# Kernel optimization log

Hardware: AMD Instinct MI355X
Metric: run time of the kernel (lower is better)

## Reference

```python
import jax, jax.numpy as jnp
import numpy as np

# AlphaFold2-scale config
C_S, C_Z, H, D = 256, 128, 8, 32
T = H * D  # total_dim = 256
B, S, N = 1, 128, 256  # batch, MSA rows, residues
EPS = 1e-5
SCALE = 1.0 / np.sqrt(D).astype(np.float32)


def _layer_norm(x, w, b):
    m = jnp.mean(x, axis=-1, keepdims=True)
    v = jnp.var(x, axis=-1, keepdims=True)
    return (x - m) * jax.lax.rsqrt(v + EPS) * w + b


def setup_inputs() -> dict:
    key = jax.random.key(0)
    ks = jax.random.split(key, 8)
    w = lambda k, shape: jax.random.normal(k, shape, dtype=jnp.float32) * 0.02
    return {
        "msa_representation": jax.random.normal(ks[0], (B, S, N, C_S), dtype=jnp.float32),
        "pair_representation": jax.random.normal(ks[1], (B, N, N, C_Z), dtype=jnp.float32),
        "ln_msa_w": jnp.ones((C_S,), jnp.float32),
        "ln_msa_b": jnp.zeros((C_S,), jnp.float32),
        "ln_pair_w": jnp.ones((C_Z,), jnp.float32),
        "ln_pair_b": jnp.zeros((C_Z,), jnp.float32),
        "Wq": w(ks[2], (C_S, T)),
        "Wk": w(ks[3], (C_S, T)),
        "Wv": w(ks[4], (C_S, T)),
        "Wpair": w(ks[5], (C_Z, H)),
        "Wg": w(ks[6], (C_S, T)),
        "bg": jnp.zeros((T,), jnp.float32),
        "Wo": w(ks[7], (T, C_S)),
        "bo": jnp.zeros((C_S,), jnp.float32),
    }


def reference(msa_representation, pair_representation, ln_msa_w, ln_msa_b,
              ln_pair_w, ln_pair_b, Wq, Wk, Wv, Wpair, Wg, bg, Wo, bo):
    msa = _layer_norm(msa_representation, ln_msa_w, ln_msa_b)  # [B,S,N,C_S]
    q = (msa @ Wq).reshape(B, S, N, H, D)
    k = (msa @ Wk).reshape(B, S, N, H, D)
    v = (msa @ Wv).reshape(B, S, N, H, D)
    g = jax.nn.sigmoid(msa @ Wg + bg).reshape(B, S, N, H, D)

    pair = _layer_norm(pair_representation, ln_pair_w, ln_pair_b)  # [B,N,N,C_Z]
    bias = jnp.transpose(pair @ Wpair, (0, 3, 1, 2))[:, None]  # [B,1,H,N,N]

    scores = jnp.einsum('bsihd,bsjhd->bshij', q, k) * SCALE + bias  # [B,S,H,N,N]
    attn = jax.nn.softmax(scores, axis=-1)
    vals = jnp.einsum('bshij,bsjhd->bsihd', attn, v)  # [B,S,N,H,D]
    vals = (g * vals).reshape(B, S, N, T)
    return vals @ Wo + bo  # [B,S,N,C_S]
```

## Files before the change

### kernel.cpp

```cpp
#include <hip/hip_runtime.h>

typedef unsigned short u16;
typedef unsigned int u32;
typedef __bf16 bf16x8 __attribute__((ext_vector_type(8)));
typedef float f32x4 __attribute__((ext_vector_type(4)));

#define EPS 1e-5f
#define SCALE 0.17677669529663687f

__device__ __forceinline__ u16 f2bf(float f) {
  u32 u = __builtin_bit_cast(u32, f);
  u32 r = (u + 0x7fffu + ((u >> 16) & 1u)) >> 16;
  return (u16)r;
}
__device__ __forceinline__ float bf2f(u16 v) {
  return __builtin_bit_cast(float, (u32)v << 16);
}
__device__ __forceinline__ u32 pack2(float a, float b) {
  return (u32)f2bf(a) | ((u32)f2bf(b) << 16);
}

__global__ __launch_bounds__(256) void k_ln_msa(const float* __restrict__ x,
                                                const float* __restrict__ w,
                                                const float* __restrict__ b,
                                                u16* __restrict__ y) {
  int wid = threadIdx.x >> 6, lane = threadIdx.x & 63;
  long row = (long)blockIdx.x * 4 + wid;
  const float4 v = *reinterpret_cast<const float4*>(x + row * 256 + lane * 4);
  float s = v.x + v.y + v.z + v.w;
  float ss = v.x * v.x + v.y * v.y + v.z * v.z + v.w * v.w;
#pragma unroll
  for (int off = 1; off < 64; off <<= 1) {
    s += __shfl_xor(s, off);
    ss += __shfl_xor(ss, off);
  }
  float m = s * (1.0f / 256.0f);
  float var = ss * (1.0f / 256.0f) - m * m;
  float rs = rsqrtf(var + EPS);
  int c = lane * 4;
  u16 o0 = f2bf((v.x - m) * rs * w[c + 0] + b[c + 0]);
  u16 o1 = f2bf((v.y - m) * rs * w[c + 1] + b[c + 1]);
  u16 o2 = f2bf((v.z - m) * rs * w[c + 2] + b[c + 2]);
  u16 o3 = f2bf((v.w - m) * rs * w[c + 3] + b[c + 3]);
  uint2 pk;
  pk.x = (u32)o0 | ((u32)o1 << 16);
  pk.y = (u32)o2 | ((u32)o3 << 16);
  *reinterpret_cast<uint2*>(y + row * 256 + c) = pk;
}

__global__ __launch_bounds__(256) void k_pair_bias(const float* __restrict__ x,
                                                   const float* __restrict__ w,
                                                   const float* __restrict__ b,
                                                   const float* __restrict__ Wp,
                                                   float* __restrict__ bias) {
  int wid = threadIdx.x >> 6, lane = threadIdx.x & 63;
  long row = (long)blockIdx.x * 4 + wid;
  const float2 v = *reinterpret_cast<const float2*>(x + row * 128 + lane * 2);
  float s = v.x + v.y, ss = v.x * v.x + v.y * v.y;
#pragma unroll
  for (int off = 1; off < 64; off <<= 1) {
    s += __shfl_xor(s, off);
    ss += __shfl_xor(ss, off);
  }
  float m = s * (1.0f / 128.0f);
  float var = ss * (1.0f / 128.0f) - m * m;
  float rs = rsqrtf(var + EPS);
  int c = lane * 2;
  float x0 = (v.x - m) * rs * w[c] + b[c];
  float x1 = (v.y - m) * rs * w[c + 1] + b[c + 1];
  const float4* wp = reinterpret_cast<const float4*>(Wp + (long)c * 8);
  float4 a0 = wp[0], a1 = wp[1], a2 = wp[2], a3 = wp[3];
  float p[8];
  p[0] = x0 * a0.x + x1 * a2.x; p[1] = x0 * a0.y + x1 * a2.y;
  p[2] = x0 * a0.z + x1 * a2.z; p[3] = x0 * a0.w + x1 * a2.w;
  p[4] = x0 * a1.x + x1 * a3.x; p[5] = x0 * a1.y + x1 * a3.y;
  p[6] = x0 * a1.z + x1 * a3.z; p[7] = x0 * a1.w + x1 * a3.w;
#pragma unroll
  for (int off = 1; off < 64; off <<= 1) {
#pragma unroll
    for (int h = 0; h < 8; h++) p[h] += __shfl_xor(p[h], off);
  }
  if (lane == 0) {
#pragma unroll
    for (int h = 0; h < 8; h++) bias[(long)h * 65536 + row] = p[h];
  }
}

__global__ __launch_bounds__(256) void k_prep_w(const float* __restrict__ Wq,
                                                const float* __restrict__ Wk,
                                                const float* __restrict__ Wv,
                                                const float* __restrict__ Wg,
                                                const float* __restrict__ Wo,
                                                u16* __restrict__ Wt,
                                                u16* __restrict__ WoT) {
  int tid = blockIdx.x * 256 + threadIdx.x;
  if (tid < 262144) {
    int n = tid >> 8, kk = tid & 255;
    int sel = n >> 8, c = n & 255;
    const float* W = (sel == 0) ? Wq : (sel == 1) ? Wk : (sel == 2) ? Wv : Wg;
    float v = W[kk * 256 + c];
    if (sel == 0) v *= SCALE;
    Wt[tid] = f2bf(v);
  } else {
    int t = tid - 262144;
    int n = t >> 8, kk = t & 255;
    WoT[t] = f2bf(Wo[kk * 256 + n]);
  }
}

__global__ __launch_bounds__(256) void k_proj(const u16* __restrict__ X,
                                              const u16* __restrict__ Wt,
                                              const float* __restrict__ bg,
                                              u16* __restrict__ qkg,
                                              u16* __restrict__ vt) {
  __shared__ u16 Bs[128 * 256];
  int tid = threadIdx.x;
  int wid = tid >> 6, lane = tid & 63;
  int lr = lane & 15, lg = lane >> 4;
  int m0 = blockIdx.x * 128;
  int n0 = blockIdx.y * 128;
  int sel = n0 >> 8;

#pragma unroll
  for (int i = 0; i < 16; i++) {
    int u = i * 256 + tid;
    int n = u >> 5, cu = u & 31;
    uint4 xw = *reinterpret_cast<const uint4*>(Wt + (long)(n0 + n) * 256 + cu * 8);
    *reinterpret_cast<uint4*>(&Bs[n * 256 + ((cu ^ (n & 7)) * 8)]) = xw;
  }
  __syncthreads();

  int mw = m0 + wid * 32;
  bf16x8 a[2][8];
#pragma unroll
  for (int mi = 0; mi < 2; mi++)
#pragma unroll
    for (int kk = 0; kk < 8; kk++)
      a[mi][kk] = *reinterpret_cast<const bf16x8*>(
          X + (long)(mw + mi * 16 + lr) * 256 + kk * 32 + lg * 8);

  f32x4 acc[2][8];
#pragma unroll
  for (int mi = 0; mi < 2; mi++)
#pragma unroll
    for (int ni = 0; ni < 8; ni++) acc[mi][ni] = (f32x4){0.f, 0.f, 0.f, 0.f};

#pragma unroll
  for (int ni = 0; ni < 8; ni++) {
    bf16x8 bfr[8];
#pragma unroll
    for (int kk = 0; kk < 8; kk++)
      bfr[kk] = *reinterpret_cast<const bf16x8*>(
          &Bs[(ni * 16 + lr) * 256 + (((kk * 4 + lg) ^ (lr & 7)) * 8)]);
#pragma unroll
    for (int kk = 0; kk < 8; kk++) {
      acc[0][ni] = __builtin_amdgcn_mfma_f32_16x16x32_bf16(a[0][kk], bfr[kk], acc[0][ni], 0, 0, 0);
      acc[1][ni] = __builtin_amdgcn_mfma_f32_16x16x32_bf16(a[1][kk], bfr[kk], acc[1][ni], 0, 0, 0);
    }
  }

  int s = m0 >> 8;
  if (sel == 2) {
#pragma unroll
    for (int ni = 0; ni < 8; ni++) {
      int cq = (n0 & 255) + ni * 16 + lr;
      int hh = cq >> 5, dd = cq & 31;
      u16* vbase = vt + (((long)s * 8 + hh) * 32 + dd) * 256;
#pragma unroll
      for (int mi = 0; mi < 2; mi++) {
        int i = (m0 & 255) + wid * 32 + mi * 16 + lg * 4;
        uint2 pk;
        pk.x = pack2(acc[mi][ni][0], acc[mi][ni][1]);
        pk.y = pack2(acc[mi][ni][2], acc[mi][ni][3]);
        *reinterpret_cast<uint2*>(vbase + i) = pk;
      }
    }
  } else {
    int t = (sel == 3) ? 2 : sel;
#pragma unroll
    for (int ni = 0; ni < 8; ni++) {
      int cq = (n0 & 255) + ni * 16 + lr;
      int hh = cq >> 5, dd = cq & 31;
      float bgv = (sel == 3) ? bg[cq] : 0.f;
      u16* qbase = qkg + (long)(t * 8 + hh) * 32768 * 32;
#pragma unroll
      for (int mi = 0; mi < 2; mi++) {
#pragma unroll
        for (int r = 0; r < 4; r++) {
          int row = m0 + wid * 32 + mi * 16 + lg * 4 + r;
          float val = acc[mi][ni][r];
          if (sel == 3) val = 1.0f / (1.0f + __expf(-(val + bgv)));
          qbase[(long)row * 32 + dd] = f2bf(val);
        }
      }
    }
  }
}

__global__ __launch_bounds__(256) void k_attn(const u16* __restrict__ qkg,
                                              const u16* __restrict__ vt,
                                              const float* __restrict__ bias,
                                              u16* __restrict__ vals) {
  __shared__ alignas(16) u16 VTs[32 * 272];
  __shared__ alignas(16) u16 Plds[4][16 * 272];
  int tid = threadIdx.x;
  int wid = tid >> 6, lane = tid & 63;
  int lr = lane & 15, lg = lane >> 4;
  int i0 = blockIdx.x * 64, h = blockIdx.y, s = blockIdx.z;

  const u16* qb = qkg + ((long)(0 + h) * 32768 + s * 256) * 32;
  const u16* kb = qkg + ((long)(8 + h) * 32768 + s * 256) * 32;
  const u16* gb = qkg + ((long)(16 + h) * 32768 + s * 256) * 32;
  const u16* vb = vt + ((long)s * 8 + h) * 32 * 256;

#pragma unroll
  for (int k = 0; k < 4; k++) {
    int c = tid + k * 256;
    uint4 u = *reinterpret_cast<const uint4*>(vb + c * 8);
    int d = c >> 5, p = c & 31;
    *reinterpret_cast<uint4*>(&VTs[d * 272 + p * 8]) = u;
  }
  __syncthreads();

  int iw0 = i0 + wid * 16;
  bf16x8 qf = *reinterpret_cast<const bf16x8*>(qb + (long)(iw0 + lr) * 32 + lg * 8);

  f32x4 p[16];
#pragma unroll
  for (int jt = 0; jt < 16; jt++) {
    bf16x8 kf = *reinterpret_cast<const bf16x8*>(kb + (long)(jt * 16 + lr) * 32 + lg * 8);
    f32x4 z = (f32x4){0.f, 0.f, 0.f, 0.f};
    p[jt] = __builtin_amdgcn_mfma_f32_16x16x32_bf16(kf, qf, z, 0, 0, 0);
  }

  const float4* bp4 = reinterpret_cast<const float4*>(bias + (long)h * 65536 + (long)(iw0 + lr) * 256);
  float sum = 0.f;
#pragma unroll
  for (int jt = 0; jt < 16; jt++) {
    float4 bv = bp4[jt * 4 + lg];
    float e0 = __expf(p[jt][0] + bv.x);
    float e1 = __expf(p[jt][1] + bv.y);
    float e2 = __expf(p[jt][2] + bv.z);
    float e3 = __expf(p[jt][3] + bv.w);
    sum += (e0 + e1) + (e2 + e3);
    uint2 pk;
    pk.x = pack2(e0, e1);
    pk.y = pack2(e2, e3);
    *reinterpret_cast<uint2*>(&Plds[wid][lr * 272 + jt * 16 + lg * 4]) = pk;
  }
  sum += __shfl_xor(sum, 16);
  sum += __shfl_xor(sum, 32);

  f32x4 o[2];
  o[0] = (f32x4){0.f, 0.f, 0.f, 0.f};
  o[1] = (f32x4){0.f, 0.f, 0.f, 0.f};
#pragma unroll
  for (int ks = 0; ks < 8; ks++) {
    bf16x8 pa = *reinterpret_cast<const bf16x8*>(&Plds[wid][lr * 272 + ks * 32 + lg * 8]);
#pragma unroll
    for (int nt = 0; nt < 2; nt++) {
      bf16x8 vf = *reinterpret_cast<const bf16x8*>(&VTs[(nt * 16 + lr) * 272 + ks * 32 + lg * 8]);
      o[nt] = __builtin_amdgcn_mfma_f32_16x16x32_bf16(pa, vf, o[nt], 0, 0, 0);
    }
  }

  float inv = 1.0f / sum;
#pragma unroll
  for (int r = 0; r < 4; r++) {
    float invr = __shfl(inv, lg * 4 + r);
    int row = iw0 + lg * 4 + r;
#pragma unroll
    for (int nt = 0; nt < 2; nt++) {
      int d = nt * 16 + lr;
      float gv = bf2f(gb[(long)row * 32 + d]);
      float ov = o[nt][r] * invr * gv;
      vals[((long)s * 256 + row) * 256 + h * 32 + d] = f2bf(ov);
    }
  }
}

__global__ __launch_bounds__(256) void k_out(const u16* __restrict__ X,
                                             const u16* __restrict__ WoT,
                                             const float* __restrict__ bo,
                                             float* __restrict__ out) {
  __shared__ u16 Bs[128 * 256];
  int tid = threadIdx.x;
  int wid = tid >> 6, lane = tid & 63;
  int lr = lane & 15, lg = lane >> 4;
  int m0 = blockIdx.x * 128;
  int n0 = blockIdx.y * 128;

#pragma unroll
  for (int i = 0; i < 16; i++) {
    int u = i * 256 + tid;
    int n = u >> 5, cu = u & 31;
    uint4 xw = *reinterpret_cast<const uint4*>(WoT + (long)(n0 + n) * 256 + cu * 8);
    *reinterpret_cast<uint4*>(&Bs[n * 256 + ((cu ^ (n & 7)) * 8)]) = xw;
  }
  __syncthreads();

  int mw = m0 + wid * 32;
  bf16x8 a[2][8];
#pragma unroll
  for (int mi = 0; mi < 2; mi++)
#pragma unroll
    for (int kk = 0; kk < 8; kk++)
      a[mi][kk] = *reinterpret_cast<const bf16x8*>(
          X + (long)(mw + mi * 16 + lr) * 256 + kk * 32 + lg * 8);

  f32x4 acc[2][8];
#pragma unroll
  for (int mi = 0; mi < 2; mi++)
#pragma unroll
    for (int ni = 0; ni < 8; ni++) acc[mi][ni] = (f32x4){0.f, 0.f, 0.f, 0.f};

#pragma unroll
  for (int ni = 0; ni < 8; ni++) {
    bf16x8 bfr[8];
#pragma unroll
    for (int kk = 0; kk < 8; kk++)
      bfr[kk] = *reinterpret_cast<const bf16x8*>(
          &Bs[(ni * 16 + lr) * 256 + (((kk * 4 + lg) ^ (lr & 7)) * 8)]);
#pragma unroll
    for (int kk = 0; kk < 8; kk++) {
      acc[0][ni] = __builtin_amdgcn_mfma_f32_16x16x32_bf16(a[0][kk], bfr[kk], acc[0][ni], 0, 0, 0);
      acc[1][ni] = __builtin_amdgcn_mfma_f32_16x16x32_bf16(a[1][kk], bfr[kk], acc[1][ni], 0, 0, 0);
    }
  }

#pragma unroll
  for (int ni = 0; ni < 8; ni++) {
    int col = n0 + ni * 16 + lr;
    float bias_c = bo[col];
#pragma unroll
    for (int mi = 0; mi < 2; mi++) {
#pragma unroll
      for (int r = 0; r < 4; r++) {
        int row = m0 + wid * 32 + mi * 16 + lg * 4 + r;
        out[(long)row * 256 + col] = acc[mi][ni][r] + bias_c;
      }
    }
  }
}

extern "C" void kernel_launch(void* const* d_in, const int* in_sizes, int n_in,
                              void* d_out, int out_size, void* d_ws, size_t ws_size,
                              hipStream_t stream) {
  (void)in_sizes; (void)n_in; (void)out_size; (void)ws_size;
  const float* msa = (const float*)d_in[0];
  const float* pair = (const float*)d_in[1];
  const float* ln_msa_w = (const float*)d_in[2];
  const float* ln_msa_b = (const float*)d_in[3];
  const float* ln_pair_w = (const float*)d_in[4];
  const float* ln_pair_b = (const float*)d_in[5];
  const float* Wq = (const float*)d_in[6];
  const float* Wk = (const float*)d_in[7];
  const float* Wv = (const float*)d_in[8];
  const float* Wpair = (const float*)d_in[9];
  const float* Wg = (const float*)d_in[10];
  const float* bg = (const float*)d_in[11];
  const float* Wo = (const float*)d_in[12];
  const float* bo = (const float*)d_in[13];
  float* out = (float*)d_out;

  char* ws = (char*)d_ws;
  u16* msa_ln = (u16*)(ws + 0);
  u16* qkg    = (u16*)(ws + 16777216);
  u16* vt     = (u16*)(ws + 67108864);
  float* bias = (float*)(ws + 83886080);
  u16* vals   = (u16*)(ws + 85983232);
  u16* Wt     = (u16*)(ws + 102760448);
  u16* WoT    = (u16*)(ws + 103284736);

  k_prep_w<<<dim3(1280), dim3(256), 0, stream>>>(Wq, Wk, Wv, Wg, Wo, Wt, WoT);
  k_ln_msa<<<dim3(8192), dim3(256), 0, stream>>>(msa, ln_msa_w, ln_msa_b, msa_ln);
  k_pair_bias<<<dim3(16384), dim3(256), 0, stream>>>(pair, ln_pair_w, ln_pair_b, Wpair, bias);
  k_proj<<<dim3(256, 8), dim3(256), 0, stream>>>(msa_ln, Wt, bg, qkg, vt);
  k_attn<<<dim3(4, 8, 128), dim3(256), 0, stream>>>(qkg, vt, bias, vals);
  k_out<<<dim3(256, 2), dim3(256), 0, stream>>>(vals, WoT, bo, out);
}
```

Measured before the change: 173.8 us.

## Swizzle attention LDS tiles, split softmax/PV into halves, vectorize gated output

Replaces padded LDS rows for V^T and P with XOR-swizzled layouts, halving the P buffer by processing the 256 keys in two halves that each write P and immediately run the PV MFMAs. The MFMA operands are swapped so the output fragment lands transposed, which lets each lane read gate values and write outputs as packed 4-element vectors instead of scalar bf16 stores with shuffles. The aim is fewer LDS bank conflicts, less shared memory per block for occupancy, and coalesced stores. Correctness depends on the swizzle indices matching between writes and reads.

```diff
diff --git a/kernel.cpp b/kernel.cpp
--- a/kernel.cpp
+++ b/kernel.cpp
@@ -201,8 +201,8 @@
                                               const u16* __restrict__ vt,
                                               const float* __restrict__ bias,
                                               u16* __restrict__ vals) {
-  __shared__ alignas(16) u16 VTs[32 * 272];
-  __shared__ alignas(16) u16 Plds[4][16 * 272];
+  __shared__ alignas(16) u16 VTs[32 * 256];
+  __shared__ alignas(16) u16 Plds[4][16 * 128];
   int tid = threadIdx.x;
   int wid = tid >> 6, lane = tid & 63;
   int lr = lane & 15, lg = lane >> 4;
@@ -216,9 +216,9 @@
 #pragma unroll
   for (int k = 0; k < 4; k++) {
     int c = tid + k * 256;
-    uint4 u = *reinterpret_cast<const uint4*>(vb + c * 8);
-    int d = c >> 5, p = c & 31;
-    *reinterpret_cast<uint4*>(&VTs[d * 272 + p * 8]) = u;
+    uint4 u4 = *reinterpret_cast<const uint4*>(vb + c * 8);
+    int d = c >> 5, pp = c & 31;
+    *reinterpret_cast<uint4*>(&VTs[d * 256 + ((pp ^ (d & 7)) * 8)]) = u4;
   }
   __syncthreads();
 
@@ -235,47 +235,56 @@
 
   const float4* bp4 = reinterpret_cast<const float4*>(bias + (long)h * 65536 + (long)(iw0 + lr) * 256);
   float sum = 0.f;
-#pragma unroll
-  for (int jt = 0; jt < 16; jt++) {
-    float4 bv = bp4[jt * 4 + lg];
-    float e0 = __expf(p[jt][0] + bv.x);
-    float e1 = __expf(p[jt][1] + bv.y);
-    float e2 = __expf(p[jt][2] + bv.z);
-    float e3 = __expf(p[jt][3] + bv.w);
-    sum += (e0 + e1) + (e2 + e3);
-    uint2 pk;
-    pk.x = pack2(e0, e1);
-    pk.y = pack2(e2, e3);
-    *reinterpret_cast<uint2*>(&Plds[wid][lr * 272 + jt * 16 + lg * 4]) = pk;
-  }
-  sum += __shfl_xor(sum, 16);
-  sum += __shfl_xor(sum, 32);
-
   f32x4 o[2];
   o[0] = (f32x4){0.f, 0.f, 0.f, 0.f};
   o[1] = (f32x4){0.f, 0.f, 0.f, 0.f};
-#pragma unroll
-  for (int ks = 0; ks < 8; ks++) {
-    bf16x8 pa = *reinterpret_cast<const bf16x8*>(&Plds[wid][lr * 272 + ks * 32 + lg * 8]);
-#pragma unroll
-    for (int nt = 0; nt < 2; nt++) {
-      bf16x8 vf = *reinterpret_cast<const bf16x8*>(&VTs[(nt * 16 + lr) * 272 + ks * 32 + lg * 8]);
-      o[nt] = __builtin_amdgcn_mfma_f32_16x16x32_bf16(pa, vf, o[nt], 0, 0, 0);
-    }
-  }
+
+#pragma unroll
+  for (int half = 0; half < 2; half++) {
+#pragma unroll
+    for (int jt8 = 0; jt8 < 8; jt8++) {
+      int jt = half * 8 + jt8;
+      float4 bv = bp4[jt * 4 + lg];
+      float e0 = __expf(p[jt][0] + bv.x);
+      float e1 = __expf(p[jt][1] + bv.y);
+      float e2 = __expf(p[jt][2] + bv.z);
+      float e3 = __expf(p[jt][3] + bv.w);
+      sum += (e0 + e1) + (e2 + e3);
+      int u = (jt8 * 2 + (lg >> 1)) ^ (lr & 7);
+      uint2 pk;
+      pk.x = pack2(e0, e1);
+      pk.y = pack2(e2, e3);
+      *reinterpret_cast<uint2*>(&Plds[wid][lr * 128 + u * 8 + (lg & 1) * 4]) = pk;
+    }
+#pragma unroll
+    for (int ks4 = 0; ks4 < 4; ks4++) {
+      int ks = half * 4 + ks4;
+      int pu = (ks4 * 4 + lg) ^ (lr & 7);
+      bf16x8 pa = *reinterpret_cast<const bf16x8*>(&Plds[wid][lr * 128 + pu * 8]);
+#pragma unroll
+      for (int nt = 0; nt < 2; nt++) {
+        int vu = (ks * 4 + lg) ^ (lr & 7);
+        bf16x8 vf = *reinterpret_cast<const bf16x8*>(&VTs[(nt * 16 + lr) * 256 + vu * 8]);
+        o[nt] = __builtin_amdgcn_mfma_f32_16x16x32_bf16(vf, pa, o[nt], 0, 0, 0);
+      }
+    }
+  }
+
+  sum += __shfl_xor(sum, 16);
+  sum += __shfl_xor(sum, 32);
 
   float inv = 1.0f / sum;
-#pragma unroll
-  for (int r = 0; r < 4; r++) {
-    float invr = __shfl(inv, lg * 4 + r);
-    int row = iw0 + lg * 4 + r;
-#pragma unroll
-    for (int nt = 0; nt < 2; nt++) {
-      int d = nt * 16 + lr;
-      float gv = bf2f(gb[(long)row * 32 + d]);
-      float ov = o[nt][r] * invr * gv;
-      vals[((long)s * 256 + row) * 256 + h * 32 + d] = f2bf(ov);
-    }
+  int row = iw0 + lr;
+#pragma unroll
+  for (int nt = 0; nt < 2; nt++) {
+    int d0 = nt * 16 + lg * 4;
+    uint2 gv = *reinterpret_cast<const uint2*>(gb + (long)row * 32 + d0);
+    float g0 = bf2f((u16)(gv.x & 0xffff)), g1 = bf2f((u16)(gv.x >> 16));
+    float g2 = bf2f((u16)(gv.y & 0xffff)), g3 = bf2f((u16)(gv.y >> 16));
+    uint2 st;
+    st.x = pack2(o[nt][0] * inv * g0, o[nt][1] * inv * g1);
+    st.y = pack2(o[nt][2] * inv * g2, o[nt][3] * inv * g3);
+    *reinterpret_cast<uint2*>(&vals[((long)s * 256 + row) * 256 + h * 32 + d0]) = st;
   }
 }
 
```

After: 186.8 us. +7.5%, slower.
